# Kernel tuning notes

Measured on AMD Instinct MI355X. Metric: run time of the kernel, lower is better.

## Reference

```python
import jax, jax.numpy as jnp
import numpy as np

D_MODEL = 1024
NHEAD = 16
HEAD_DIM = D_MODEL // NHEAD


def setup_inputs() -> dict:
    key = jax.random.key(0)
    ks = jax.random.split(key, 11)
    B, S = 2, 2048
    s = 1.0 / np.sqrt(D_MODEL)
    return {
        "query": jax.random.normal(ks[0], (B, S, D_MODEL), jnp.float32),
        "key": jax.random.normal(ks[1], (B, S, D_MODEL), jnp.float32),
        "value": jax.random.normal(ks[2], (B, S, D_MODEL), jnp.float32),
        "wq_w": jax.random.normal(ks[3], (D_MODEL, D_MODEL), jnp.float32) * s,
        "wq_b": jax.random.normal(ks[4], (D_MODEL,), jnp.float32) * s,
        "wk_w": jax.random.normal(ks[5], (D_MODEL, D_MODEL), jnp.float32) * s,
        "wk_b": jax.random.normal(ks[6], (D_MODEL,), jnp.float32) * s,
        "wv_w": jax.random.normal(ks[7], (D_MODEL, D_MODEL), jnp.float32) * s,
        "wv_b": jax.random.normal(ks[8], (D_MODEL,), jnp.float32) * s,
        "wo_w": jax.random.normal(ks[9], (D_MODEL, D_MODEL), jnp.float32) * s,
        "wo_b": jax.random.normal(ks[10], (D_MODEL,), jnp.float32) * s,
    }


def reference(query, key, value, wq_w, wq_b, wk_w, wk_b, wv_w, wv_b, wo_w, wo_b):
    B, S, _ = query.shape
    # torch Linear: x @ W.T + b
    def proj(x, w, b):
        y = x @ w.T + b
        return y.reshape(B, S, NHEAD, HEAD_DIM).transpose(0, 2, 1, 3)  # [B,H,S,Dh]

    Q = proj(query, wq_w, wq_b)
    K = proj(key, wk_w, wk_b)
    V = proj(value, wv_w, wv_b)

    scale = 1.0 / np.sqrt(HEAD_DIM).astype(np.float32)
    scores = jnp.einsum("bhqd,bhkd->bhqk", Q, K) * scale  # [B,H,S,S]
    causal = jnp.tril(jnp.ones((S, S), dtype=bool))
    scores = jnp.where(causal, scores, -jnp.inf)
    attn = jax.nn.softmax(scores, axis=-1)
    out = jnp.einsum("bhqk,bhkd->bhqd", attn, V)  # [B,H,S,Dh]
    out = out.transpose(0, 2, 1, 3).reshape(B, S, D_MODEL)
    return out @ wo_w.T + wo_b
```

## Files before the change

kernel.cpp:

```cpp
#include <hip/hip_runtime.h>
#include <stdint.h>

#define D_MODEL 1024
#define S_LEN   2048
#define NHEAD   16
#define HEAD_DIM 64
#define BATCH   2
#define M_TOT   (BATCH * S_LEN)
#define Q_SCALE 0.18033688011112042f

using bf16x8 = __attribute__((ext_vector_type(8))) short;
using f32x4  = __attribute__((ext_vector_type(4))) float;

__device__ __forceinline__ unsigned short f2bf(float f) {
  union { float f; unsigned int u; } v; v.f = f;
  unsigned int u = v.u;
  return (unsigned short)((u + 0x7FFFu + ((u >> 16) & 1u)) >> 16);
}
__device__ __forceinline__ unsigned int pkbf(float a, float b) {
#if __has_builtin(__builtin_amdgcn_cvt_pk_bf16_f32)
  auto p = __builtin_amdgcn_cvt_pk_bf16_f32(a, b);
  union { decltype(p) v; unsigned int u; } c; c.v = p;
  return c.u;
#else
  return (unsigned int)f2bf(a) | ((unsigned int)f2bf(b) << 16);
#endif
}
__device__ __forceinline__ bf16x8 cvt8(const float* p) {
  const float4 a = *(const float4*)p;
  const float4 b = *(const float4*)(p + 4);
  union { unsigned int u[4]; bf16x8 v; } r;
  r.u[0] = pkbf(a.x, a.y); r.u[1] = pkbf(a.z, a.w);
  r.u[2] = pkbf(b.x, b.y); r.u[3] = pkbf(b.z, b.w);
  return r.v;
}
__device__ __forceinline__ float fexp2(float x) {
#if __has_builtin(__builtin_amdgcn_exp2f)
  return __builtin_amdgcn_exp2f(x);
#else
  return __expf(x * 0.69314718055994531f);
#endif
}
__device__ __forceinline__ void async16(const unsigned short* g, short* l) {
  __builtin_amdgcn_global_load_lds(
      reinterpret_cast<const __attribute__((address_space(1))) unsigned int*>(
          reinterpret_cast<uintptr_t>(g)),
      reinterpret_cast<__attribute__((address_space(3))) unsigned int*>(
          reinterpret_cast<uintptr_t>(l)),
      16, 0, 0);
}

__device__ __forceinline__ void waitv2() {
  asm volatile("s_waitcnt vmcnt(2)" ::: "memory");
  __builtin_amdgcn_sched_barrier(0);
}
__device__ __forceinline__ void waitv3() {
  asm volatile("s_waitcnt vmcnt(3)" ::: "memory");
  __builtin_amdgcn_sched_barrier(0);
}
__device__ __forceinline__ void waitv0() {
  asm volatile("s_waitcnt vmcnt(0)" ::: "memory");
  __builtin_amdgcn_sched_barrier(0);
}
__device__ __forceinline__ void waitl0() {
  asm volatile("s_waitcnt lgkmcnt(0)" ::: "memory");
  __builtin_amdgcn_sched_barrier(0);
}

__device__ __forceinline__ void swap32(unsigned int& x, unsigned int& y) {
#if __has_builtin(__builtin_amdgcn_permlane32_swap)
  auto r = __builtin_amdgcn_permlane32_swap(x, y, false, false);
  x = (unsigned int)r[0]; y = (unsigned int)r[1];
#else
  const int lane = threadIdx.x & 63;
  unsigned int sx = (unsigned int)__shfl_xor((int)x, 32);
  unsigned int sy = (unsigned int)__shfl_xor((int)y, 32);
  unsigned int nx = (lane & 32) ? sy : x;
  unsigned int ny = (lane & 32) ? y : sx;
  x = nx; y = ny;
#endif
}
__device__ __forceinline__ void swap16(unsigned int& x, unsigned int& y) {
#if __has_builtin(__builtin_amdgcn_permlane16_swap)
  auto r = __builtin_amdgcn_permlane16_swap(x, y, false, false);
  x = (unsigned int)r[0]; y = (unsigned int)r[1];
#else
  const int lane = threadIdx.x & 63;
  unsigned int sx = (unsigned int)__shfl_xor((int)x, 16);
  unsigned int sy = (unsigned int)__shfl_xor((int)y, 16);
  unsigned int nx = (lane & 16) ? sy : x;
  unsigned int ny = (lane & 16) ? y : sx;
  x = nx; y = ny;
#endif
}

#define LDK 40

__global__ __launch_bounds__(256)
void cast_all(const float* __restrict__ wq, const float* __restrict__ wk,
              const float* __restrict__ wv, const float* __restrict__ wo,
              const float* __restrict__ q, const float* __restrict__ k,
              const float* __restrict__ v,
              unsigned short* __restrict__ wb,
              unsigned short* __restrict__ qb, unsigned short* __restrict__ kb,
              unsigned short* __restrict__ vb)
{
  const int z = blockIdx.y;
  const float* src;
  unsigned short* d;
  size_t n;
  switch (z) {
    case 0: src = wq; d = wb;                                   n = (size_t)D_MODEL * D_MODEL; break;
    case 1: src = wk; d = wb + (size_t)1 * D_MODEL * D_MODEL;   n = (size_t)D_MODEL * D_MODEL; break;
    case 2: src = wv; d = wb + (size_t)2 * D_MODEL * D_MODEL;   n = (size_t)D_MODEL * D_MODEL; break;
    case 3: src = wo; d = wb + (size_t)3 * D_MODEL * D_MODEL;   n = (size_t)D_MODEL * D_MODEL; break;
    case 4: src = q;  d = qb;                                   n = (size_t)M_TOT * D_MODEL;   break;
    case 5: src = k;  d = kb;                                   n = (size_t)M_TOT * D_MODEL;   break;
    default: src = v; d = vb;                                   n = (size_t)M_TOT * D_MODEL;   break;
  }
  const size_t i = ((size_t)blockIdx.x * 256 + threadIdx.x) * 8;
  if (i < n) *(bf16x8*)(d + i) = cvt8(src + i);
}

#define QBUF (128 * 32)

__device__ __forceinline__ void gemm_tile_cv(const unsigned short* __restrict__ A,
                                             const unsigned short* __restrict__ W,
                                             int m0, int n0,
                                             short* As, short* Bs,
                                             f32x4 acc[4][2])
{
  const int t    = threadIdx.x;
  const int lane = t & 63;
  const int w    = t >> 6;
  const int quad = lane >> 4;
  const int l16  = lane & 15;
  const int wm   = (w >> 2) * 64;
  const int wn   = (w & 3) * 32;
  const int srow = t >> 2;
  const int sc   = t & 3;
  const int scg  = (sc ^ ((srow >> 1) & 3)) * 8;
  const int sdst = srow * 32 + sc * 8;
  const int rk   = (l16 >> 1) & 3;

  const unsigned short* Ag = A + (size_t)(m0 + srow) * D_MODEL + scg;
  const unsigned short* Wg = W + (size_t)(n0 + srow) * D_MODEL + scg;

  for (int mt = 0; mt < 4; ++mt)
    for (int nt = 0; nt < 2; ++nt)
      acc[mt][nt] = f32x4{0.f, 0.f, 0.f, 0.f};

  async16(Ag,      As + sdst);
  async16(Wg,      Bs + sdst);
  async16(Ag + 32, As + QBUF + sdst);
  async16(Wg + 32, Bs + QBUF + sdst);
  waitv2();
  __builtin_amdgcn_s_barrier();

  const int cidx = (0 ^ rk);
  (void)cidx;
  int rc = 0;
  const int rq = (quad ^ rk) * 8;
  for (int kt = 0; kt < 32; ++kt) {
    const short* ab = As + rc * QBUF;
    const short* bb = Bs + rc * QBUF;
    bf16x8 af[4], bfr[2];
#pragma unroll
    for (int mt = 0; mt < 4; ++mt)
      af[mt] = *(const bf16x8*)(ab + (wm + mt * 16 + l16) * 32 + rq);
#pragma unroll
    for (int nt = 0; nt < 2; ++nt)
      bfr[nt] = *(const bf16x8*)(bb + (wn + nt * 16 + l16) * 32 + rq);

    const bool more = (kt + 2 < 32);
    if (more) {
      const int wcIdx = (rc + 2 >= 3) ? rc - 1 : rc + 2;
      const int kc = (kt + 2) * 32;
      async16(Ag + kc, As + wcIdx * QBUF + sdst);
      async16(Wg + kc, Bs + wcIdx * QBUF + sdst);
    }

    waitl0();

    __builtin_amdgcn_s_setprio(1);
#pragma unroll
    for (int mt = 0; mt < 4; ++mt)
#pragma unroll
      for (int nt = 0; nt < 2; ++nt)
        acc[mt][nt] = __builtin_amdgcn_mfma_f32_16x16x32_bf16(af[mt], bfr[nt], acc[mt][nt], 0, 0, 0);
    __builtin_amdgcn_s_setprio(0);

    if (kt < 31) {
      if (more) waitv2();
      else      waitv0();
      __builtin_amdgcn_s_barrier();
    }
    rc = (rc == 2) ? 0 : rc + 1;
  }
}

#define OBA (64 * 32)
#define OBB (128 * 32)

__device__ __forceinline__ void gemm_tile_cv64(const unsigned short* __restrict__ A,
                                               const unsigned short* __restrict__ W,
                                               int m0, int n0,
                                               short* As, short* Bs,
                                               f32x4 acc[2][4])
{
  const int t    = threadIdx.x;
  const int lane = t & 63;
  const int w    = t >> 6;
  const int quad = lane >> 4;
  const int l16  = lane & 15;
  const int wm   = (w >> 1) * 32;
  const int wn   = (w & 1) * 64;
  const int srow = t >> 2;
  const int sc   = t & 3;
  const int scg  = (sc ^ ((srow >> 1) & 3)) * 8;
  const int sdst = srow * 32 + sc * 8;
  const int rk   = (l16 >> 1) & 3;
  const int rq   = (quad ^ rk) * 8;

  const unsigned short* Ag  = A + (size_t)(m0 + srow)      * D_MODEL + scg;
  const unsigned short* Wg0 = W + (size_t)(n0 + srow)      * D_MODEL + scg;
  const unsigned short* Wg1 = W + (size_t)(n0 + 64 + srow) * D_MODEL + scg;

  for (int mt = 0; mt < 2; ++mt)
    for (int nt = 0; nt < 4; ++nt)
      acc[mt][nt] = f32x4{0.f, 0.f, 0.f, 0.f};

  async16(Ag,       As + sdst);
  async16(Wg0,      Bs + sdst);
  async16(Wg1,      Bs + OBA + sdst);
  async16(Ag + 32,  As + OBA + sdst);
  async16(Wg0 + 32, Bs + OBB + sdst);
  async16(Wg1 + 32, Bs + OBB + OBA + sdst);
  waitv3();
  __builtin_amdgcn_s_barrier();

  int rc = 0;
  for (int kt = 0; kt < 32; ++kt) {
    const short* ab = As + rc * OBA;
    const short* bb = Bs + rc * OBB;
    bf16x8 af[2], bfr[4];
#pragma unroll
    for (int mt = 0; mt < 2; ++mt)
      af[mt] = *(const bf16x8*)(ab + (wm + mt * 16 + l16) * 32 + rq);
#pragma unroll
    for (int nt = 0; nt < 4; ++nt)
      bfr[nt] = *(const bf16x8*)(bb + (wn + nt * 16 + l16) * 32 + rq);

    const bool more = (kt + 2 < 32);
    if (more) {
      const int wcIdx = (rc + 2 >= 3) ? rc - 1 : rc + 2;
      const int kc = (kt + 2) * 32;
      async16(Ag + kc,  As + wcIdx * OBA + sdst);
      async16(Wg0 + kc, Bs + wcIdx * OBB + sdst);
      async16(Wg1 + kc, Bs + wcIdx * OBB + OBA + sdst);
    }

    waitl0();

    __builtin_amdgcn_s_setprio(1);
#pragma unroll
    for (int mt = 0; mt < 2; ++mt)
#pragma unroll
      for (int nt = 0; nt < 4; ++nt)
        acc[mt][nt] = __builtin_amdgcn_mfma_f32_16x16x32_bf16(af[mt], bfr[nt], acc[mt][nt], 0, 0, 0);
    __builtin_amdgcn_s_setprio(0);

    if (kt < 31) {
      if (more) waitv3();
      else      waitv0();
      __builtin_amdgcn_s_barrier();
    }
    rc = (rc == 2) ? 0 : rc + 1;
  }
}

__device__ __forceinline__ void gemm_tile_f32(const float* __restrict__ A,
                                              const unsigned short* __restrict__ W,
                                              int m0, int n0,
                                              short* As, short* Bs,
                                              f32x4 acc[4][4])
{
  const int t    = threadIdx.x;
  const int lane = t & 63;
  const int w    = t >> 6;
  const int quad = lane >> 4;
  const int l16  = lane & 15;
  const int wm   = (w >> 1) * 64;
  const int wn   = (w & 1) * 64;
  const int srow = t >> 2;
  const int scol = (t & 3) * 8;

  for (int mt = 0; mt < 4; ++mt)
    for (int nt = 0; nt < 4; ++nt)
      acc[mt][nt] = f32x4{0.f, 0.f, 0.f, 0.f};

  for (int kt = 0; kt < D_MODEL / 32; ++kt) {
    const int kc = kt * 32 + scol;
    const bf16x8 a0 = cvt8(A + (size_t)(m0 + srow)      * D_MODEL + kc);
    const bf16x8 a1 = cvt8(A + (size_t)(m0 + srow + 64) * D_MODEL + kc);
    const bf16x8 b0 = *(const bf16x8*)(W + (size_t)(n0 + srow)      * D_MODEL + kc);
    const bf16x8 b1 = *(const bf16x8*)(W + (size_t)(n0 + srow + 64) * D_MODEL + kc);
    __syncthreads();
    *(bf16x8*)(As + (srow)      * LDK + scol) = a0;
    *(bf16x8*)(As + (srow + 64) * LDK + scol) = a1;
    *(bf16x8*)(Bs + (srow)      * LDK + scol) = b0;
    *(bf16x8*)(Bs + (srow + 64) * LDK + scol) = b1;
    __syncthreads();

    bf16x8 af[4], bfr[4];
    for (int mt = 0; mt < 4; ++mt)
      af[mt] = *(const bf16x8*)(As + (wm + mt * 16 + l16) * LDK + quad * 8);
    for (int nt = 0; nt < 4; ++nt)
      bfr[nt] = *(const bf16x8*)(Bs + (wn + nt * 16 + l16) * LDK + quad * 8);
    for (int mt = 0; mt < 4; ++mt)
      for (int nt = 0; nt < 4; ++nt)
        acc[mt][nt] = __builtin_amdgcn_mfma_f32_16x16x32_bf16(af[mt], bfr[nt], acc[mt][nt], 0, 0, 0);
  }
}

__device__ __forceinline__ void qkv_epilogue8w(int z, int m0, int n0,
                                               const float* __restrict__ bias,
                                               float scale,
                                               unsigned short* __restrict__ dst,
                                               f32x4 acc[4][2])
{
  const int t    = threadIdx.x;
  const int lane = t & 63;
  const int w    = t >> 6;
  const int quad = lane >> 4;
  const int l16  = lane & 15;
  const int wm   = (w >> 2) * 64;
  const int wn   = (w & 3) * 32;

  for (int nt = 0; nt < 2; ++nt) {
    const int n = n0 + wn + nt * 16 + l16;
    const float bb = bias[n];
    const int h = n >> 6, d = n & 63;
    for (int mt = 0; mt < 4; ++mt) {
      for (int r = 0; r < 4; ++r) {
        const int m = m0 + wm + mt * 16 + quad * 4 + r;
        const int b = m >> 11, s = m & 2047;
        const unsigned short val = f2bf((acc[mt][nt][r] + bb) * scale);
        if (z < 2)
          dst[((size_t)((b * NHEAD + h) * S_LEN + s)) * HEAD_DIM + d] = val;
        else
          dst[((size_t)((b * NHEAD + h) * HEAD_DIM + d)) * S_LEN + s] = val;
      }
    }
  }
}

__global__ __launch_bounds__(512)
void qkv_fast(const unsigned short* __restrict__ qb,
              const unsigned short* __restrict__ kb,
              const unsigned short* __restrict__ vb,
              const unsigned short* __restrict__ wqb,
              const unsigned short* __restrict__ wkb,
              const unsigned short* __restrict__ wvb,
              const float* __restrict__ bq, const float* __restrict__ bk,
              const float* __restrict__ bv,
              unsigned short* __restrict__ Qh, unsigned short* __restrict__ Kh,
              unsigned short* __restrict__ VhT)
{
  __shared__ __attribute__((aligned(16))) short As[3 * QBUF];
  __shared__ __attribute__((aligned(16))) short Bs[3 * QBUF];
  const int z = blockIdx.z;
  const unsigned short* A    = (z == 0) ? qb  : (z == 1) ? kb  : vb;
  const unsigned short* W    = (z == 0) ? wqb : (z == 1) ? wkb : wvb;
  const float*          bias = (z == 0) ? bq  : (z == 1) ? bk  : bv;
  unsigned short*       dst  = (z == 0) ? Qh  : (z == 1) ? Kh  : VhT;
  const float           scale = (z == 0) ? Q_SCALE : 1.0f;

  const int m0 = blockIdx.x * 128, n0 = blockIdx.y * 128;
  f32x4 acc[4][2];
  gemm_tile_cv(A, W, m0, n0, As, Bs, acc);
  qkv_epilogue8w(z, m0, n0, bias, scale, dst, acc);
}

__global__ __launch_bounds__(256)
void qkv_slow(const float* __restrict__ query, const float* __restrict__ key,
              const float* __restrict__ value,
              const unsigned short* __restrict__ wqb,
              const unsigned short* __restrict__ wkb,
              const unsigned short* __restrict__ wvb,
              const float* __restrict__ bq, const float* __restrict__ bk,
              const float* __restrict__ bv,
              unsigned short* __restrict__ Qh, unsigned short* __restrict__ Kh,
              unsigned short* __restrict__ VhT)
{
  __shared__ __attribute__((aligned(16))) short As[128 * LDK];
  __shared__ __attribute__((aligned(16))) short Bs[128 * LDK];
  const int z = blockIdx.z;
  const float*          A    = (z == 0) ? query : (z == 1) ? key : value;
  const unsigned short* W    = (z == 0) ? wqb   : (z == 1) ? wkb : wvb;
  const float*          bias = (z == 0) ? bq    : (z == 1) ? bk  : bv;
  unsigned short*       dst  = (z == 0) ? Qh    : (z == 1) ? Kh  : VhT;
  const float           scale = (z == 0) ? Q_SCALE : 1.0f;

  const int m0 = blockIdx.x * 128, n0 = blockIdx.y * 128;
  f32x4 acc[4][4];
  gemm_tile_f32(A, W, m0, n0, As, Bs, acc);

  const int t    = threadIdx.x;
  const int lane = t & 63;
  const int w    = t >> 6;
  const int quad = lane >> 4;
  const int l16  = lane & 15;
  const int wm   = (w >> 1) * 64;
  const int wn   = (w & 1) * 64;
  for (int nt = 0; nt < 4; ++nt) {
    const int n = n0 + wn + nt * 16 + l16;
    const float bb = bias[n];
    const int h = n >> 6, d = n & 63;
    for (int mt = 0; mt < 4; ++mt) {
      for (int r = 0; r < 4; ++r) {
        const int m = m0 + wm + mt * 16 + quad * 4 + r;
        const int b = m >> 11, s = m & 2047;
        const unsigned short val = f2bf((acc[mt][nt][r] + bb) * scale);
        if (z < 2)
          dst[((size_t)((b * NHEAD + h) * S_LEN + s)) * HEAD_DIM + d] = val;
        else
          dst[((size_t)((b * NHEAD + h) * HEAD_DIM + d)) * S_LEN + s] = val;
      }
    }
  }
}

__global__ __launch_bounds__(256)
void out_proj(const unsigned short* __restrict__ Oh,
              const unsigned short* __restrict__ wob,
              const float* __restrict__ bo,
              float* __restrict__ dst)
{
  __shared__ __attribute__((aligned(16))) short As[3 * OBA];
  __shared__ __attribute__((aligned(16))) short Bs[3 * OBB];
  const int m0 = blockIdx.x * 64, n0 = blockIdx.y * 128;
  f32x4 acc[2][4];
  gemm_tile_cv64(Oh, wob, m0, n0, As, Bs, acc);

  const int t    = threadIdx.x;
  const int lane = t & 63;
  const int w    = t >> 6;
  const int quad = lane >> 4;
  const int l16  = lane & 15;
  const int wm   = (w >> 1) * 32;
  const int wn   = (w & 1) * 64;

  for (int nt = 0; nt < 4; ++nt) {
    const int n = n0 + wn + nt * 16 + l16;
    const float bb = bo[n];
    for (int mt = 0; mt < 2; ++mt)
      for (int r = 0; r < 4; ++r) {
        const int m = m0 + wm + mt * 16 + quad * 4 + r;
        dst[(size_t)m * D_MODEL + n] = acc[mt][nt][r] + bb;
      }
  }
}

struct Frags { bf16x8 ka0, ka1, kb0, kb1, v0, v1, v2, v3; };
struct StageRegs { bf16x8 k0, k1, v0, v1; };

#define KS_LD 72
#define VT_LD 136

__device__ __forceinline__ StageRegs load_stage(const unsigned short* __restrict__ Kb,
                                                const unsigned short* __restrict__ Vb,
                                                int k0, int kr, int kc, int vd, int vc) {
  StageRegs r;
  r.k0 = *(const bf16x8*)(Kb + (size_t)(k0 + kr)      * HEAD_DIM + kc);
  r.k1 = *(const bf16x8*)(Kb + (size_t)(k0 + kr + 64) * HEAD_DIM + kc);
  r.v0 = *(const bf16x8*)(Vb + (size_t)(vd)      * S_LEN + k0 + vc);
  r.v1 = *(const bf16x8*)(Vb + (size_t)(vd + 32) * S_LEN + k0 + vc);
  return r;
}
__device__ __forceinline__ void write_stage(const StageRegs& r, short* Ks, short* Vts,
                                            int kr, int kc, int vd, int vc) {
  *(bf16x8*)(Ks + (kr)      * KS_LD + kc) = r.k0;
  *(bf16x8*)(Ks + (kr + 64) * KS_LD + kc) = r.k1;
  *(bf16x8*)(Vts + (vd)      * VT_LD + vc) = r.v0;
  *(bf16x8*)(Vts + (vd + 32) * VT_LD + vc) = r.v1;
}
__device__ __forceinline__ Frags lds_frags(const short* Ks, const short* Vts,
                                           int c, int quad, int l16) {
  Frags f;
  const short* kp = Ks + (c * 32 + l16) * KS_LD + quad * 8;
  f.ka0 = *(const bf16x8*)(kp);
  f.ka1 = *(const bf16x8*)(kp + 32);
  f.kb0 = *(const bf16x8*)(kp + 16 * KS_LD);
  f.kb1 = *(const bf16x8*)(kp + 16 * KS_LD + 32);
  const short* vp = Vts + l16 * VT_LD + c * 32 + quad * 8;
  f.v0 = *(const bf16x8*)(vp);
  f.v1 = *(const bf16x8*)(vp + 16 * VT_LD);
  f.v2 = *(const bf16x8*)(vp + 32 * VT_LD);
  f.v3 = *(const bf16x8*)(vp + 48 * VT_LD);
  return f;
}

template <int MODE>
__device__ __forceinline__ void proc_chunk(const Frags& f, const bf16x8 qf[2],
                                           const bf16x8& ones, int quad, int l16,
                                           f32x4& lacc, f32x4 oacc[4]) {
  f32x4 s0 = f32x4{0.f, 0.f, 0.f, 0.f};
  f32x4 s1 = f32x4{0.f, 0.f, 0.f, 0.f};
  __builtin_amdgcn_s_setprio(1);
  s0 = __builtin_amdgcn_mfma_f32_16x16x32_bf16(f.ka0, qf[0], s0, 0, 0, 0);
  s0 = __builtin_amdgcn_mfma_f32_16x16x32_bf16(f.ka1, qf[1], s0, 0, 0, 0);
  if (MODE != 1) {
    s1 = __builtin_amdgcn_mfma_f32_16x16x32_bf16(f.kb0, qf[0], s1, 0, 0, 0);
    s1 = __builtin_amdgcn_mfma_f32_16x16x32_bf16(f.kb1, qf[1], s1, 0, 0, 0);
  }
  __builtin_amdgcn_s_setprio(0);

  float st0[4], st1[4];
  const int kl = quad * 4;
#pragma unroll
  for (int r = 0; r < 4; ++r) {
    if (MODE == 0) {
      st0[r] = fexp2(s0[r]);
      st1[r] = fexp2(s1[r]);
    } else if (MODE == 1) {
      st0[r] = (kl + r <= l16) ? fexp2(s0[r]) : 0.f;
      st1[r] = 0.f;
    } else {
      st0[r] = fexp2(s0[r]);
      st1[r] = (kl + r <= l16) ? fexp2(s1[r]) : 0.f;
    }
  }

  unsigned int a = pkbf(st0[0], st0[1]), b = pkbf(st0[2], st0[3]);
  unsigned int c = pkbf(st1[0], st1[1]), e = pkbf(st1[2], st1[3]);
  swap32(a, c); swap32(b, e);
  swap16(a, c); swap16(b, e);
  union { unsigned int u[4]; bf16x8 v; } pf;
  pf.u[0] = a; pf.u[1] = b; pf.u[2] = c; pf.u[3] = e;

  __builtin_amdgcn_s_setprio(1);
  lacc = __builtin_amdgcn_mfma_f32_16x16x32_bf16(pf.v, ones, lacc, 0, 0, 0);
  oacc[0] = __builtin_amdgcn_mfma_f32_16x16x32_bf16(pf.v, f.v0, oacc[0], 0, 0, 0);
  oacc[1] = __builtin_amdgcn_mfma_f32_16x16x32_bf16(pf.v, f.v1, oacc[1], 0, 0, 0);
  oacc[2] = __builtin_amdgcn_mfma_f32_16x16x32_bf16(pf.v, f.v2, oacc[2], 0, 0, 0);
  oacc[3] = __builtin_amdgcn_mfma_f32_16x16x32_bf16(pf.v, f.v3, oacc[3], 0, 0, 0);
  __builtin_amdgcn_s_setprio(0);
}

__global__ __launch_bounds__(512, 4)
void attn_kernel(const unsigned short* __restrict__ Qh,
                 const unsigned short* __restrict__ Kh,
                 const unsigned short* __restrict__ VhT,
                 unsigned short* __restrict__ O)
{
  __shared__ __attribute__((aligned(16))) short Ks[2][128 * KS_LD];
  __shared__ __attribute__((aligned(16))) short Vts[2][64 * VT_LD];

  const int orig = blockIdx.x;
  const int xcd  = orig & 7;
  const int li   = orig >> 3;
  const int bh   = xcd * 4 + (li & 3);
  const int j16  = li >> 2;
  const int qt   = (j16 < 8) ? (15 - j16) : (j16 - 8);
  const int q0   = qt * 128;
  const int b    = bh >> 4;
  const int h    = bh & 15;
  const int t    = threadIdx.x;
  const int w    = t >> 6;
  const int lane = t & 63;
  const int quad = lane >> 4;
  const int l16  = lane & 15;
  const int rowbase = q0 + w * 16;

  const unsigned short* Kb = Kh + (size_t)bh * S_LEN * HEAD_DIM;
  const unsigned short* Vb = VhT + (size_t)bh * HEAD_DIM * S_LEN;
  const int kr = t >> 3, kc = (t & 7) * 8;
  const int vd = t >> 4, vc = (t & 15) * 8;

  bf16x8 qf[2];
  {
    const size_t qrow = (size_t)bh * S_LEN + rowbase + l16;
    qf[0] = *(const bf16x8*)(Qh + qrow * HEAD_DIM + quad * 8);
    qf[1] = *(const bf16x8*)(Qh + qrow * HEAD_DIM + 32 + quad * 8);
  }
  bf16x8 ones;
#pragma unroll
  for (int j = 0; j < 8; ++j) ones[j] = (short)0x3F80;

  f32x4 lacc = f32x4{0.f, 0.f, 0.f, 0.f};
  f32x4 oacc[4];
#pragma unroll
  for (int dt = 0; dt < 4; ++dt) oacc[dt] = f32x4{0.f, 0.f, 0.f, 0.f};

  const int nT = qt + 1;
  const int cw = w >> 1;
  const bool odd = (w & 1) != 0;

  StageRegs rs = load_stage(Kb, Vb, 0, kr, kc, vd, vc);
  write_stage(rs, Ks[0], Vts[0], kr, kc, vd, vc);
  __syncthreads();
  for (int j = 0; j < nT; ++j) {
    const short* Ksj = (j & 1) ? Ks[1] : Ks[0];
    const short* Vtj = (j & 1) ? Vts[1] : Vts[0];
    short* Ksn = (j & 1) ? Ks[0] : Ks[1];
    short* Vtn = (j & 1) ? Vts[0] : Vts[1];
    const bool more = (j + 1 < nT);
    if (more) rs = load_stage(Kb, Vb, (j + 1) * 128, kr, kc, vd, vc);
    if (j < qt) {
#pragma unroll
      for (int c = 0; c < 4; ++c) {
        const Frags f = lds_frags(Ksj, Vtj, c, quad, l16);
        proc_chunk<0>(f, qf, ones, quad, l16, lacc, oacc);
      }
    } else {
      for (int c = 0; c < cw; ++c) {
        const Frags f = lds_frags(Ksj, Vtj, c, quad, l16);
        proc_chunk<0>(f, qf, ones, quad, l16, lacc, oacc);
      }
      const Frags f = lds_frags(Ksj, Vtj, cw, quad, l16);
      if (odd) proc_chunk<2>(f, qf, ones, quad, l16, lacc, oacc);
      else     proc_chunk<1>(f, qf, ones, quad, l16, lacc, oacc);
    }
    if (more) write_stage(rs, Ksn, Vtn, kr, kc, vd, vc);
    __syncthreads();
  }

#pragma unroll
  for (int dt = 0; dt < 4; ++dt)
#pragma unroll
    for (int r = 0; r < 4; ++r) {
      const int rowg = rowbase + quad * 4 + r;
      O[(size_t)(b * S_LEN + rowg) * D_MODEL + h * 64 + dt * 16 + l16] =
          f2bf(oacc[dt][r] / lacc[r]);
    }
}

extern "C" void kernel_launch(void* const* d_in, const int* in_sizes, int n_in,
                              void* d_out, int out_size, void* d_ws, size_t ws_size,
                              hipStream_t stream)
{
  (void)in_sizes; (void)n_in; (void)out_size;
  const float* q  = (const float*)d_in[0];
  const float* k  = (const float*)d_in[1];
  const float* v  = (const float*)d_in[2];
  const float* wq = (const float*)d_in[3];
  const float* bq = (const float*)d_in[4];
  const float* wk = (const float*)d_in[5];
  const float* bk = (const float*)d_in[6];
  const float* wv = (const float*)d_in[7];
  const float* bv = (const float*)d_in[8];
  const float* wo = (const float*)d_in[9];
  const float* bo = (const float*)d_in[10];
  float* out = (float*)d_out;

  unsigned short* wb  = (unsigned short*)d_ws;
  unsigned short* wqb = wb;
  unsigned short* wkb = wb + (size_t)1 * D_MODEL * D_MODEL;
  unsigned short* wvb = wb + (size_t)2 * D_MODEL * D_MODEL;
  unsigned short* wob = wb + (size_t)3 * D_MODEL * D_MODEL;
  unsigned short* Kh  = wb + (size_t)4 * D_MODEL * D_MODEL;
  unsigned short* VhT = Kh + (size_t)M_TOT * D_MODEL;
  unsigned short* Oh  = VhT + (size_t)M_TOT * D_MODEL;
  unsigned short* qb  = Oh;
  unsigned short* vb  = Oh + (size_t)M_TOT * D_MODEL;
  unsigned short* Qh  = (unsigned short*)d_out;
  unsigned short* kb  = Qh + (size_t)M_TOT * D_MODEL;

  const bool fast = ws_size >= (size_t)40 * 1024 * 1024;

  if (fast) {
    dim3 gc((size_t)M_TOT * D_MODEL / (256 * 8), 7, 1);
    cast_all<<<gc, 256, 0, stream>>>(wq, wk, wv, wo, q, k, v, wb, qb, kb, vb);
    dim3 g1(M_TOT / 128, D_MODEL / 128, 3);
    qkv_fast<<<g1, 512, 0, stream>>>(qb, kb, vb, wqb, wkb, wvb, bq, bk, bv, Qh, Kh, VhT);
  } else {
    dim3 gc((size_t)D_MODEL * D_MODEL / (256 * 8), 4, 1);
    cast_all<<<gc, 256, 0, stream>>>(wq, wk, wv, wo, q, k, v, wb, qb, kb, vb);
    dim3 g1(M_TOT / 128, D_MODEL / 128, 3);
    qkv_slow<<<g1, 256, 0, stream>>>(q, k, v, wqb, wkb, wvb, bq, bk, bv, Qh, Kh, VhT);
  }

  dim3 g2(512, 1, 1);
  attn_kernel<<<g2, 512, 0, stream>>>(Qh, Kh, VhT, Oh);

  dim3 g3(M_TOT / 64, D_MODEL / 128, 1);
  out_proj<<<g3, 256, 0, stream>>>(Oh, wob, bo, out);
}
```

Before: 205.7 us.

## Split attention key chunks across warp pairs with two query row blocks per warp

Each warp now handles 32 query rows (two 16-row units) but only half of the four 32-key chunks per tile. Partial output and row-sum accumulators are then combined across the warp pair through shared memory before normalising. Each K/V fragment read from LDS now feeds two query units, which cuts LDS traffic per MFMA and spreads the causal diagonal work more evenly across warps. In exchange it doubles the per-warp accumulator and Q registers under the same 512x4 launch bounds, which risks spills or lower occupancy, and it adds an extra barrier plus an LDS reduction at the end.

After: 222.6 us. +8.2%, slower.

```diff
diff --git a/kernel.cpp b/kernel.cpp
--- a/kernel.cpp
+++ b/kernel.cpp
@@ -142,6 +142,7 @@
   const int scg  = (sc ^ ((srow >> 1) & 3)) * 8;
   const int sdst = srow * 32 + sc * 8;
   const int rk   = (l16 >> 1) & 3;
+  const int rq   = (quad ^ rk) * 8;
 
   const unsigned short* Ag = A + (size_t)(m0 + srow) * D_MODEL + scg;
   const unsigned short* Wg = W + (size_t)(n0 + srow) * D_MODEL + scg;
@@ -157,10 +158,7 @@
   waitv2();
   __builtin_amdgcn_s_barrier();
 
-  const int cidx = (0 ^ rk);
-  (void)cidx;
   int rc = 0;
-  const int rq = (quad ^ rk) * 8;
   for (int kt = 0; kt < 32; ++kt) {
     const short* ab = As + rc * QBUF;
     const short* bb = Bs + rc * QBUF;
@@ -548,6 +546,14 @@
   __builtin_amdgcn_s_setprio(0);
 }
 
+__device__ __forceinline__ void proc_unit(const Frags& f, const bf16x8 qf[2],
+                                          const bf16x8& ones, int quad, int l16,
+                                          int du, f32x4& lacc, f32x4 oacc[4]) {
+  if (du >= 32)      proc_chunk<0>(f, qf, ones, quad, l16, lacc, oacc);
+  else if (du == 16) proc_chunk<2>(f, qf, ones, quad, l16, lacc, oacc);
+  else               proc_chunk<1>(f, qf, ones, quad, l16, lacc, oacc);
+}
+
 __global__ __launch_bounds__(512, 4)
 void attn_kernel(const unsigned short* __restrict__ Qh,
                  const unsigned short* __restrict__ Kh,
@@ -571,32 +577,37 @@
   const int lane = t & 63;
   const int quad = lane >> 4;
   const int l16  = lane & 15;
-  const int rowbase = q0 + w * 16;
+  const int qq   = w >> 1;
+  const int kh   = w & 1;
+  const int rb0  = q0 + qq * 32;
+  const int rb1  = rb0 + 16;
 
   const unsigned short* Kb = Kh + (size_t)bh * S_LEN * HEAD_DIM;
   const unsigned short* Vb = VhT + (size_t)bh * HEAD_DIM * S_LEN;
   const int kr = t >> 3, kc = (t & 7) * 8;
   const int vd = t >> 4, vc = (t & 15) * 8;
 
-  bf16x8 qf[2];
-  {
-    const size_t qrow = (size_t)bh * S_LEN + rowbase + l16;
-    qf[0] = *(const bf16x8*)(Qh + qrow * HEAD_DIM + quad * 8);
-    qf[1] = *(const bf16x8*)(Qh + qrow * HEAD_DIM + 32 + quad * 8);
+  bf16x8 qf[2][2];
+#pragma unroll
+  for (int u = 0; u < 2; ++u) {
+    const size_t qrow = (size_t)bh * S_LEN + rb0 + u * 16 + l16;
+    qf[u][0] = *(const bf16x8*)(Qh + qrow * HEAD_DIM + quad * 8);
+    qf[u][1] = *(const bf16x8*)(Qh + qrow * HEAD_DIM + 32 + quad * 8);
   }
   bf16x8 ones;
 #pragma unroll
   for (int j = 0; j < 8; ++j) ones[j] = (short)0x3F80;
 
-  f32x4 lacc = f32x4{0.f, 0.f, 0.f, 0.f};
-  f32x4 oacc[4];
-#pragma unroll
-  for (int dt = 0; dt < 4; ++dt) oacc[dt] = f32x4{0.f, 0.f, 0.f, 0.f};
+  f32x4 lacc[2];
+  f32x4 oacc[2][4];
+  lacc[0] = f32x4{0.f, 0.f, 0.f, 0.f};
+  lacc[1] = f32x4{0.f, 0.f, 0.f, 0.f};
+#pragma unroll
+  for (int u = 0; u < 2; ++u)
+#pragma unroll
+    for (int dt = 0; dt < 4; ++dt) oacc[u][dt] = f32x4{0.f, 0.f, 0.f, 0.f};
 
   const int nT = qt + 1;
-  const int cw = w >> 1;
-  const bool odd = (w & 1) != 0;
-
   StageRegs rs = load_stage(Kb, Vb, 0, kr, kc, vd, vc);
   write_stage(rs, Ks[0], Vts[0], kr, kc, vd, vc);
   __syncthreads();
@@ -607,33 +618,55 @@
     short* Vtn = (j & 1) ? Vts[0] : Vts[1];
     const bool more = (j + 1 < nT);
     if (more) rs = load_stage(Kb, Vb, (j + 1) * 128, kr, kc, vd, vc);
-    if (j < qt) {
-#pragma unroll
-      for (int c = 0; c < 4; ++c) {
+#pragma unroll
+    for (int cc = 0; cc < 2; ++cc) {
+      const int c   = 2 * kh + cc;
+      const int k0c = j * 128 + c * 32;
+      const int du1 = rb1 - k0c;
+      if (du1 >= 0) {
         const Frags f = lds_frags(Ksj, Vtj, c, quad, l16);
-        proc_chunk<0>(f, qf, ones, quad, l16, lacc, oacc);
+        proc_unit(f, qf[1], ones, quad, l16, du1, lacc[1], oacc[1]);
+        const int du0 = rb0 - k0c;
+        if (du0 >= 0)
+          proc_unit(f, qf[0], ones, quad, l16, du0, lacc[0], oacc[0]);
       }
-    } else {
-      for (int c = 0; c < cw; ++c) {
-        const Frags f = lds_frags(Ksj, Vtj, c, quad, l16);
-        proc_chunk<0>(f, qf, ones, quad, l16, lacc, oacc);
-      }
-      const Frags f = lds_frags(Ksj, Vtj, cw, quad, l16);
-      if (odd) proc_chunk<2>(f, qf, ones, quad, l16, lacc, oacc);
-      else     proc_chunk<1>(f, qf, ones, quad, l16, lacc, oacc);
     }
     if (more) write_stage(rs, Ksn, Vtn, kr, kc, vd, vc);
     __syncthreads();
   }
 
-#pragma unroll
-  for (int dt = 0; dt < 4; ++dt)
-#pragma unroll
-    for (int r = 0; r < 4; ++r) {
-      const int rowg = rowbase + quad * 4 + r;
-      O[(size_t)(b * S_LEN + rowg) * D_MODEL + h * 64 + dt * 16 + l16] =
-          f2bf(oacc[dt][r] / lacc[r]);
-    }
+  float* redo = (float*)&Ks[0][0];
+  float* redl = (float*)&Vts[0][0];
+  if (kh == 1) {
+#pragma unroll
+    for (int u = 0; u < 2; ++u) {
+#pragma unroll
+      for (int dt = 0; dt < 4; ++dt)
+        *(f32x4*)(redo + (((qq * 2 + u) * 4 + dt) << 8) + lane * 4) = oacc[u][dt];
+      *(f32x4*)(redl + ((qq * 2 + u) << 8) + lane * 4) = lacc[u];
+    }
+  }
+  __syncthreads();
+  if (kh == 0) {
+#pragma unroll
+    for (int u = 0; u < 2; ++u) {
+#pragma unroll
+      for (int dt = 0; dt < 4; ++dt) {
+        const f32x4 p = *(const f32x4*)(redo + (((qq * 2 + u) * 4 + dt) << 8) + lane * 4);
+        oacc[u][dt] += p;
+      }
+      const f32x4 pl = *(const f32x4*)(redl + ((qq * 2 + u) << 8) + lane * 4);
+      lacc[u] += pl;
+#pragma unroll
+      for (int dt = 0; dt < 4; ++dt)
+#pragma unroll
+        for (int r = 0; r < 4; ++r) {
+          const int rowg = rb0 + u * 16 + quad * 4 + r;
+          O[(size_t)(b * S_LEN + rowg) * D_MODEL + h * 64 + dt * 16 + l16] =
+              f2bf(oacc[u][dt][r] / lacc[u][r]);
+        }
+    }
+  }
 }
 
 extern "C" void kernel_launch(void* const* d_in, const int* in_sizes, int n_in,
```
